# Performance work log

Hardware: AMD Instinct MI355X
Metric: run time of the kernel (lower is better)

The kernel has to match this reference:

```python
import math
import jax, jax.numpy as jnp
import numpy as np

B, S, D, H, L, V = 4, 1024, 1024, 16, 12, 32000
DH = D // H
MAX_LEN = 5000


def _layernorm(x, g, b, eps=1e-5):
    mu = jnp.mean(x, axis=-1, keepdims=True)
    var = jnp.mean(jnp.square(x - mu), axis=-1, keepdims=True)
    return (x - mu) * jax.lax.rsqrt(var + eps) * g + b


def _make_pe():
    pos = np.arange(MAX_LEN, dtype=np.float32)[:, None]
    div = np.exp(np.arange(0, D, 2, dtype=np.float32) * (-math.log(10000.0) / D))
    pe = np.zeros((MAX_LEN, D), dtype=np.float32)
    pe[:, 0::2] = np.sin(pos * div)
    pe[:, 1::2] = np.cos(pos * div)
    return jnp.asarray(pe[:, None, :])  # [max_len, 1, D] as in the torch buffer


def setup_inputs() -> dict:
    key = jax.random.key(0)
    ks = jax.random.split(key, 8)
    X = jax.random.randint(ks[0], (B, S), 0, V)
    emb = jax.random.normal(ks[1], (V, D), dtype=jnp.float32) * 0.02
    pe = _make_pe()
    ln1_g = jnp.ones((L, D), jnp.float32)
    ln1_b = jnp.zeros((L, D), jnp.float32)
    wa = jax.random.normal(ks[2], (L, D, 3 * D), dtype=jnp.float32) * 0.02
    ba = jnp.zeros((L, 3 * D), jnp.float32)
    wp = jax.random.normal(ks[3], (L, D, D), dtype=jnp.float32) * 0.02
    bp = jnp.zeros((L, D), jnp.float32)
    ln2_g = jnp.ones((L, D), jnp.float32)
    ln2_b = jnp.zeros((L, D), jnp.float32)
    wf = jax.random.normal(ks[4], (L, D, D), dtype=jnp.float32) * 0.02
    bf = jnp.zeros((L, D), jnp.float32)
    wout = jax.random.normal(ks[5], (V, D), dtype=jnp.float32) * 0.02
    return dict(X=X, emb=emb, pe=pe, ln1_g=ln1_g, ln1_b=ln1_b, wa=wa, ba=ba,
                wp=wp, bp=bp, ln2_g=ln2_g, ln2_b=ln2_b, wf=wf, bf=bf, wout=wout)


def _block(x, ln1g, ln1b, wa_i, ba_i, wp_i, bp_i, ln2g, ln2b, wf_i, bf_i):
    h = _layernorm(x, ln1g, ln1b)               # post-ln1 value is the residual base
    qkv = h @ wa_i + ba_i                        # [B,S,3D]
    q, k, v = jnp.split(qkv, 3, axis=-1)
    def heads(t):
        return t.reshape(B, S, H, DH).transpose(0, 2, 1, 3)  # [B,H,S,DH]
    q, k, v = heads(q), heads(k), heads(v)
    scores = jnp.einsum('bhqd,bhkd->bhqk', q, k)  # NOTE: no 1/sqrt(d) scaling (scale=False)
    probs = jax.nn.softmax(scores, axis=-1)
    o = jnp.einsum('bhqk,bhkd->bhqd', probs, v)
    o = o.transpose(0, 2, 1, 3).reshape(B, S, D)
    attn_out = o @ wp_i + bp_i
    x = h + attn_out
    x = x + _layernorm(x, ln2g, ln2b) @ wf_i + bf_i
    return x


def reference(X, emb, pe, ln1_g, ln1_b, wa, ba, wp, bp, ln2_g, ln2_b, wf, bf, wout):
    x = emb[X] * math.sqrt(D)           # [B,S,D]
    x = x + pe[:B]                       # faithful: pe indexed by batch dim, broadcast over seq
    for i in range(L):
        x = _block(x, ln1_g[i], ln1_b[i], wa[i], ba[i], wp[i], bp[i],
                   ln2_g[i], ln2_b[i], wf[i], bf[i])
    logits = jnp.einsum('bsd,vd->bsv', x, wout)  # Linear(d, vocab, bias=False)
    return logits
```

## Files before the change

### kernel.cpp

```cpp
#include <hip/hip_runtime.h>
#include <hip/hip_bf16.h>

typedef __attribute__((ext_vector_type(4))) float f32x4;
typedef __attribute__((ext_vector_type(8))) short s16x8;
typedef __attribute__((ext_vector_type(4))) short s16x4;

constexpr int Bc = 4, Sc = 1024, Dc = 1024, Hc = 16, DHc = 64, Lc = 12, Vc = 32000;
constexpr int Tc = Bc * Sc;
constexpr int D3c = 3 * Dc;

static __device__ __forceinline__ short f2bf(float f) {
  union { float f; unsigned u; } v; v.f = f;
  unsigned r = (v.u + 0x7FFFu + ((v.u >> 16) & 1u)) >> 16;
  return (short)r;
}

__launch_bounds__(256)
__global__ void k_embed(const int* __restrict__ X, const float* __restrict__ emb,
                        const float* __restrict__ pe, float* __restrict__ x) {
  int row = blockIdx.x;
  int b = row >> 10;
  int tok = X[row];
  int t = threadIdx.x;
  float4 e = ((const float4*)(emb + (size_t)tok * Dc))[t];
  float4 p = ((const float4*)(pe + (size_t)b * Dc))[t];
  float4 r;
  r.x = e.x * 32.0f + p.x;  r.y = e.y * 32.0f + p.y;
  r.z = e.z * 32.0f + p.z;  r.w = e.w * 32.0f + p.w;
  ((float4*)(x + (size_t)row * Dc))[t] = r;
}

template<bool WF32>
__launch_bounds__(256)
__global__ void k_ln(const float* __restrict__ x, const float* __restrict__ g,
                     const float* __restrict__ be, float* __restrict__ hf,
                     short* __restrict__ hb) {
  int row = blockIdx.x, t = threadIdx.x;
  float4 v = ((const float4*)(x + (size_t)row * Dc))[t];
  float s1 = v.x + v.y + v.z + v.w;
  float s2 = v.x * v.x + v.y * v.y + v.z * v.z + v.w * v.w;
#pragma unroll
  for (int off = 1; off < 64; off <<= 1) {
    s1 += __shfl_xor(s1, off);
    s2 += __shfl_xor(s2, off);
  }
  __shared__ float a1[4], a2[4];
  if ((t & 63) == 0) { a1[t >> 6] = s1; a2[t >> 6] = s2; }
  __syncthreads();
  s1 = a1[0] + a1[1] + a1[2] + a1[3];
  s2 = a2[0] + a2[1] + a2[2] + a2[3];
  float mu = s1 * (1.0f / Dc);
  float var = s2 * (1.0f / Dc) - mu * mu;
  float rs = rsqrtf(var + 1e-5f);
  float4 gg = ((const float4*)g)[t];
  float4 bb = ((const float4*)be)[t];
  float4 r;
  r.x = (v.x - mu) * rs * gg.x + bb.x;
  r.y = (v.y - mu) * rs * gg.y + bb.y;
  r.z = (v.z - mu) * rs * gg.z + bb.z;
  r.w = (v.w - mu) * rs * gg.w + bb.w;
  if (WF32) ((float4*)(hf + (size_t)row * Dc))[t] = r;
  s16x4 o; o[0] = f2bf(r.x); o[1] = f2bf(r.y); o[2] = f2bf(r.z); o[3] = f2bf(r.w);
  ((s16x4*)(hb + (size_t)row * Dc))[t] = o;
}

__launch_bounds__(256)
__global__ void k_transpose_bf(const float* __restrict__ in0, short* __restrict__ out0,
                               int R, int C) {
  const float* in = in0 + (size_t)blockIdx.z * R * C;
  short* out = out0 + (size_t)blockIdx.z * R * C;
  __shared__ float tile[64][65];
  int c0 = blockIdx.x * 64, r0 = blockIdx.y * 64;
  int t = threadIdx.x;
#pragma unroll
  for (int e = 0; e < 16; ++e) {
    int idx = e * 256 + t;
    int r = idx >> 6, c = idx & 63;
    tile[r][c] = in[(size_t)(r0 + r) * C + c0 + c];
  }
  __syncthreads();
#pragma unroll
  for (int e = 0; e < 16; ++e) {
    int idx = e * 256 + t;
    int c = idx >> 6, r = idx & 63;
    out[(size_t)(c0 + c) * R + r0 + r] = f2bf(tile[r][c]);
  }
}

__launch_bounds__(256)
__global__ void k_f2bf(const float* __restrict__ in, short* __restrict__ out, size_t n) {
  size_t i = ((size_t)blockIdx.x * 256 + threadIdx.x) * 4;
  size_t stride = (size_t)gridDim.x * 1024;
  for (; i < n; i += stride) {
    float4 v = *(const float4*)(in + i);
    s16x4 r; r[0] = f2bf(v.x); r[1] = f2bf(v.y); r[2] = f2bf(v.z); r[3] = f2bf(v.w);
    *(s16x4*)(out + i) = r;
  }
}

template<int MODE>
__launch_bounds__(256)
__global__ void k_gemm(const short* __restrict__ A, const short* __restrict__ Bt,
                       const float* __restrict__ bias, const float* __restrict__ res,
                       void* __restrict__ Cout, int M, int N, int K) {
  __shared__ __align__(16) short Al[128][40];
  __shared__ __align__(16) short Bl[128][40];
  int m0 = blockIdx.y * 128, n0 = blockIdx.x * 128;
  int t = threadIdx.x;
  int w = t >> 6, lane = t & 63;
  int wr = w >> 1, wc = w & 1;
  int lg = lane >> 4, lr = lane & 15;
  f32x4 acc[4][4];
#pragma unroll
  for (int i = 0; i < 4; ++i)
#pragma unroll
    for (int j = 0; j < 4; ++j) { acc[i][j][0] = 0.f; acc[i][j][1] = 0.f; acc[i][j][2] = 0.f; acc[i][j][3] = 0.f; }
  int srow = t >> 1, skc = (t & 1) * 16;
  const short* ga = A + (size_t)(m0 + srow) * K + skc;
  const short* gb = Bt + (size_t)(n0 + srow) * K + skc;
  for (int k0 = 0; k0 < K; k0 += 32) {
    s16x8 a0 = *(const s16x8*)(ga + k0);
    s16x8 a1 = *(const s16x8*)(ga + k0 + 8);
    s16x8 b0 = *(const s16x8*)(gb + k0);
    s16x8 b1 = *(const s16x8*)(gb + k0 + 8);
    *(s16x8*)&Al[srow][skc] = a0;
    *(s16x8*)&Al[srow][skc + 8] = a1;
    *(s16x8*)&Bl[srow][skc] = b0;
    *(s16x8*)&Bl[srow][skc + 8] = b1;
    __syncthreads();
    s16x8 af[4], bfr[4];
#pragma unroll
    for (int mi = 0; mi < 4; ++mi) af[mi] = *(const s16x8*)&Al[wr * 64 + mi * 16 + lr][lg * 8];
#pragma unroll
    for (int ni = 0; ni < 4; ++ni) bfr[ni] = *(const s16x8*)&Bl[wc * 64 + ni * 16 + lr][lg * 8];
#pragma unroll
    for (int mi = 0; mi < 4; ++mi)
#pragma unroll
      for (int ni = 0; ni < 4; ++ni)
        acc[mi][ni] = __builtin_amdgcn_mfma_f32_16x16x32_bf16(af[mi], bfr[ni], acc[mi][ni], 0, 0, 0);
    __syncthreads();
  }
#pragma unroll
  for (int mi = 0; mi < 4; ++mi) {
#pragma unroll
    for (int ni = 0; ni < 4; ++ni) {
      int ncol = n0 + wc * 64 + ni * 16 + lr;
      float bv = (MODE == 2) ? 0.0f : bias[ncol];
      int mbase = m0 + wr * 64 + mi * 16 + lg * 4;
#pragma unroll
      for (int j = 0; j < 4; ++j) {
        size_t idx = (size_t)(mbase + j) * N + ncol;
        float vv = acc[mi][ni][j] + bv;
        if (MODE == 1) vv += res[idx];
        if (MODE == 0) ((short*)Cout)[idx] = f2bf(vv);
        else           ((float*)Cout)[idx] = vv;
      }
    }
  }
}

__launch_bounds__(256)
__global__ void k_attn(const short* __restrict__ qkv, short* __restrict__ obf) {
  int bh = blockIdx.x;
  int b = bh >> 4, h = bh & 15;
  int q0 = blockIdx.y * 64;
  int t = threadIdx.x, w = t >> 6, lane = t & 63;
  int lg = lane >> 4, lr = lane & 15;
  __shared__ __align__(16) short vls[64][72];
  __shared__ __align__(16) short pls[64][72];
  s16x8 qf0, qf1;
  {
    const short* qp = qkv + (size_t)(b * Sc + q0 + w * 16 + lr) * D3c + h * DHc + lg * 8;
    qf0 = *(const s16x8*)qp;
    qf1 = *(const s16x8*)(qp + 32);
  }
  float mrow[4], lrow[4];
  f32x4 oacc[4];
#pragma unroll
  for (int j = 0; j < 4; ++j) { mrow[j] = -1e30f; lrow[j] = 0.0f; }
#pragma unroll
  for (int f = 0; f < 4; ++f) { oacc[f][0] = 0.f; oacc[f][1] = 0.f; oacc[f][2] = 0.f; oacc[f][3] = 0.f; }

  int vsk = t >> 2, vdh = (t & 3) * 16;
  const short* vbase = qkv + (size_t)(b * Sc) * D3c + 2 * Dc + h * DHc;
  const short* kbase = qkv + (size_t)(b * Sc) * D3c + Dc + h * DHc;

  for (int kt = 0; kt < Sc / 64; ++kt) {
    int k0 = kt * 64;
    __syncthreads();
    {
      const short* vp = vbase + (size_t)(k0 + vsk) * D3c + vdh;
      s16x8 v0 = *(const s16x8*)vp;
      s16x8 v1 = *(const s16x8*)(vp + 8);
#pragma unroll
      for (int e = 0; e < 8; ++e) vls[vdh + e][vsk] = v0[e];
#pragma unroll
      for (int e = 0; e < 8; ++e) vls[vdh + 8 + e][vsk] = v1[e];
    }
    __syncthreads();
    f32x4 sc[4];
#pragma unroll
    for (int f = 0; f < 4; ++f) {
      const short* kp = kbase + (size_t)(k0 + f * 16 + lr) * D3c + lg * 8;
      s16x8 kf0 = *(const s16x8*)kp;
      s16x8 kf1 = *(const s16x8*)(kp + 32);
      f32x4 c; c[0] = 0.f; c[1] = 0.f; c[2] = 0.f; c[3] = 0.f;
      c = __builtin_amdgcn_mfma_f32_16x16x32_bf16(qf0, kf0, c, 0, 0, 0);
      c = __builtin_amdgcn_mfma_f32_16x16x32_bf16(qf1, kf1, c, 0, 0, 0);
      sc[f] = c;
    }
#pragma unroll
    for (int j = 0; j < 4; ++j) {
      float mx = fmaxf(fmaxf(sc[0][j], sc[1][j]), fmaxf(sc[2][j], sc[3][j]));
#pragma unroll
      for (int off = 1; off < 16; off <<= 1) mx = fmaxf(mx, __shfl_xor(mx, off));
      float mn = fmaxf(mrow[j], mx);
      float scale = __expf(mrow[j] - mn);
      mrow[j] = mn;
      float s = 0.0f;
#pragma unroll
      for (int f = 0; f < 4; ++f) {
        float pv = __expf(sc[f][j] - mn);
        sc[f][j] = pv;
        s += pv;
      }
#pragma unroll
      for (int off = 1; off < 16; off <<= 1) s += __shfl_xor(s, off);
      lrow[j] = lrow[j] * scale + s;
#pragma unroll
      for (int f = 0; f < 4; ++f) oacc[f][j] *= scale;
    }
#pragma unroll
    for (int f = 0; f < 4; ++f)
#pragma unroll
      for (int j = 0; j < 4; ++j)
        pls[w * 16 + lg * 4 + j][f * 16 + lr] = f2bf(sc[f][j]);
    __syncthreads();
    s16x8 pa0 = *(const s16x8*)&pls[w * 16 + lr][lg * 8];
    s16x8 pa1 = *(const s16x8*)&pls[w * 16 + lr][32 + lg * 8];
#pragma unroll
    for (int f = 0; f < 4; ++f) {
      s16x8 vb0 = *(const s16x8*)&vls[f * 16 + lr][lg * 8];
      s16x8 vb1 = *(const s16x8*)&vls[f * 16 + lr][32 + lg * 8];
      oacc[f] = __builtin_amdgcn_mfma_f32_16x16x32_bf16(pa0, vb0, oacc[f], 0, 0, 0);
      oacc[f] = __builtin_amdgcn_mfma_f32_16x16x32_bf16(pa1, vb1, oacc[f], 0, 0, 0);
    }
  }
#pragma unroll
  for (int j = 0; j < 4; ++j) {
    float inv = 1.0f / lrow[j];
    int srow = q0 + w * 16 + lg * 4 + j;
#pragma unroll
    for (int f = 0; f < 4; ++f)
      obf[(size_t)(b * Sc + srow) * Dc + h * DHc + f * 16 + lr] = f2bf(oacc[f][j] * inv);
  }
}

extern "C" void kernel_launch(void* const* d_in, const int* in_sizes, int n_in,
                              void* d_out, int out_size, void* d_ws, size_t ws_size,
                              hipStream_t stream) {
  const int*   X    = (const int*)d_in[0];
  const float* emb  = (const float*)d_in[1];
  const float* pe   = (const float*)d_in[2];
  const float* ln1g = (const float*)d_in[3];
  const float* ln1b = (const float*)d_in[4];
  const float* wa   = (const float*)d_in[5];
  const float* ba   = (const float*)d_in[6];
  const float* wp   = (const float*)d_in[7];
  const float* bp   = (const float*)d_in[8];
  const float* ln2g = (const float*)d_in[9];
  const float* ln2b = (const float*)d_in[10];
  const float* wf   = (const float*)d_in[11];
  const float* bfv  = (const float*)d_in[12];
  const float* wout = (const float*)d_in[13];
  float* out = (float*)d_out;

  char* p = (char*)d_ws;
  float* x    = (float*)p; p += (size_t)Tc * Dc * 4;
  float* hx   = (float*)p; p += (size_t)Tc * Dc * 4;
  short* hbf  = (short*)p; p += (size_t)Tc * Dc * 2;
  short* l2bf = (short*)p; p += (size_t)Tc * Dc * 2;
  short* qkvb = (short*)p; p += (size_t)Tc * D3c * 2;
  short* obf  = (short*)p; p += (size_t)Tc * Dc * 2;
  short* xbf  = (short*)p; p += (size_t)Tc * Dc * 2;
  short* wat  = (short*)p; p += (size_t)Lc * D3c * Dc * 2;
  short* wpt  = (short*)p; p += (size_t)Lc * Dc * Dc * 2;
  short* wft  = (short*)p; p += (size_t)Lc * Dc * Dc * 2;
  short* woutb = (short*)p; p += (size_t)Vc * Dc * 2;

  k_transpose_bf<<<dim3(D3c / 64, Dc / 64, Lc), 256, 0, stream>>>(wa, wat, Dc, D3c);
  k_transpose_bf<<<dim3(Dc / 64, Dc / 64, Lc), 256, 0, stream>>>(wp, wpt, Dc, Dc);
  k_transpose_bf<<<dim3(Dc / 64, Dc / 64, Lc), 256, 0, stream>>>(wf, wft, Dc, Dc);
  k_f2bf<<<4096, 256, 0, stream>>>(wout, woutb, (size_t)Vc * Dc);

  k_embed<<<Tc, 256, 0, stream>>>(X, emb, pe, x);

  for (int l = 0; l < Lc; ++l) {
    k_ln<true><<<Tc, 256, 0, stream>>>(x, ln1g + l * Dc, ln1b + l * Dc, hx, hbf);
    k_gemm<0><<<dim3(D3c / 128, Tc / 128), 256, 0, stream>>>(
        hbf, wat + (size_t)l * D3c * Dc, ba + l * D3c, nullptr, qkvb, Tc, D3c, Dc);
    k_attn<<<dim3(Bc * Hc, Sc / 64), 256, 0, stream>>>(qkvb, obf);
    k_gemm<1><<<dim3(Dc / 128, Tc / 128), 256, 0, stream>>>(
        obf, wpt + (size_t)l * Dc * Dc, bp + l * Dc, hx, x, Tc, Dc, Dc);
    k_ln<false><<<Tc, 256, 0, stream>>>(x, ln2g + l * Dc, ln2b + l * Dc, nullptr, l2bf);
    k_gemm<1><<<dim3(Dc / 128, Tc / 128), 256, 0, stream>>>(
        l2bf, wft + (size_t)l * Dc * Dc, bfv + l * Dc, x, x, Tc, Dc, Dc);
  }

  k_f2bf<<<2048, 256, 0, stream>>>(x, xbf, (size_t)Tc * Dc);
  k_gemm<2><<<dim3(Vc / 128, Tc / 128), 256, 0, stream>>>(
      xbf, woutb, nullptr, nullptr, out, Tc, Vc, Dc);
}
```

Baseline: 3.672 ms.

## Use direct global-to-LDS loads, XOR-swizzled LDS, BK=64 and XCD block remap in GEMM

```diff
diff --git a/kernel.cpp b/kernel.cpp
--- a/kernel.cpp
+++ b/kernel.cpp
@@ -98,46 +98,71 @@
   }
 }
 
-template<int MODE>
+template<int MODE, bool SWZ>
 __launch_bounds__(256)
 __global__ void k_gemm(const short* __restrict__ A, const short* __restrict__ Bt,
                        const float* __restrict__ bias, const float* __restrict__ res,
-                       void* __restrict__ Cout, int M, int N, int K) {
-  __shared__ __align__(16) short Al[128][40];
-  __shared__ __align__(16) short Bl[128][40];
-  int m0 = blockIdx.y * 128, n0 = blockIdx.x * 128;
+                       void* __restrict__ Cout, int M, int N, int K, int nby) {
+  __shared__ __align__(16) short Al[128][64];
+  __shared__ __align__(16) short Bl[128][64];
+  int bid = blockIdx.x;
+  if (SWZ) {
+    int nwg = gridDim.x;
+    int q = nwg >> 3, r = nwg & 7;
+    int xcd = bid & 7, off = bid >> 3;
+    bid = (xcd < r ? xcd * (q + 1) : r * (q + 1) + (xcd - r) * q) + off;
+  }
+  int by = bid % nby;
+  int bx = bid / nby;
+  int m0 = by * 128, n0 = bx * 128;
   int t = threadIdx.x;
   int w = t >> 6, lane = t & 63;
   int wr = w >> 1, wc = w & 1;
   int lg = lane >> 4, lr = lane & 15;
+
+  int srow = t >> 3, sg = t & 7;
+  int scol = ((sg ^ (srow & 7)) * 8);
+  const short* ga = A + (size_t)(m0 + srow) * K + scol;
+  const short* gb = Bt + (size_t)(n0 + srow) * K + scol;
+  short* la = &Al[srow][sg * 8];
+  short* lb = &Bl[srow][sg * 8];
+
   f32x4 acc[4][4];
 #pragma unroll
   for (int i = 0; i < 4; ++i)
 #pragma unroll
     for (int j = 0; j < 4; ++j) { acc[i][j][0] = 0.f; acc[i][j][1] = 0.f; acc[i][j][2] = 0.f; acc[i][j][3] = 0.f; }
-  int srow = t >> 1, skc = (t & 1) * 16;
-  const short* ga = A + (size_t)(m0 + srow) * K + skc;
-  const short* gb = Bt + (size_t)(n0 + srow) * K + skc;
-  for (int k0 = 0; k0 < K; k0 += 32) {
-    s16x8 a0 = *(const s16x8*)(ga + k0);
-    s16x8 a1 = *(const s16x8*)(ga + k0 + 8);
-    s16x8 b0 = *(const s16x8*)(gb + k0);
-    s16x8 b1 = *(const s16x8*)(gb + k0 + 8);
-    *(s16x8*)&Al[srow][skc] = a0;
-    *(s16x8*)&Al[srow][skc + 8] = a1;
-    *(s16x8*)&Bl[srow][skc] = b0;
-    *(s16x8*)&Bl[srow][skc + 8] = b1;
-    __syncthreads();
-    s16x8 af[4], bfr[4];
-#pragma unroll
-    for (int mi = 0; mi < 4; ++mi) af[mi] = *(const s16x8*)&Al[wr * 64 + mi * 16 + lr][lg * 8];
-#pragma unroll
-    for (int ni = 0; ni < 4; ++ni) bfr[ni] = *(const s16x8*)&Bl[wc * 64 + ni * 16 + lr][lg * 8];
-#pragma unroll
-    for (int mi = 0; mi < 4; ++mi)
-#pragma unroll
-      for (int ni = 0; ni < 4; ++ni)
-        acc[mi][ni] = __builtin_amdgcn_mfma_f32_16x16x32_bf16(af[mi], bfr[ni], acc[mi][ni], 0, 0, 0);
+
+  for (int k0 = 0; k0 < K; k0 += 64) {
+#pragma unroll
+    for (int i = 0; i < 4; ++i) {
+      __builtin_amdgcn_global_load_lds(
+          (const __attribute__((address_space(1))) void*)(ga + (size_t)(i * 32) * K + k0),
+          (__attribute__((address_space(3))) void*)(la + i * 32 * 64), 16, 0, 0);
+      __builtin_amdgcn_global_load_lds(
+          (const __attribute__((address_space(1))) void*)(gb + (size_t)(i * 32) * K + k0),
+          (__attribute__((address_space(3))) void*)(lb + i * 32 * 64), 16, 0, 0);
+    }
+    __syncthreads();
+#pragma unroll
+    for (int kk = 0; kk < 2; ++kk) {
+      s16x8 af[4], bfr[4];
+#pragma unroll
+      for (int mi = 0; mi < 4; ++mi) {
+        int row = wr * 64 + mi * 16 + lr;
+        af[mi] = *(const s16x8*)&Al[row][((kk * 4 + lg) ^ (lr & 7)) * 8];
+      }
+#pragma unroll
+      for (int ni = 0; ni < 4; ++ni) {
+        int row = wc * 64 + ni * 16 + lr;
+        bfr[ni] = *(const s16x8*)&Bl[row][((kk * 4 + lg) ^ (lr & 7)) * 8];
+      }
+#pragma unroll
+      for (int mi = 0; mi < 4; ++mi)
+#pragma unroll
+        for (int ni = 0; ni < 4; ++ni)
+          acc[mi][ni] = __builtin_amdgcn_mfma_f32_16x16x32_bf16(af[mi], bfr[ni], acc[mi][ni], 0, 0, 0);
+    }
     __syncthreads();
   }
 #pragma unroll
@@ -295,19 +320,20 @@
 
   k_embed<<<Tc, 256, 0, stream>>>(X, emb, pe, x);
 
+  const int nby = Tc / 128;
   for (int l = 0; l < Lc; ++l) {
     k_ln<true><<<Tc, 256, 0, stream>>>(x, ln1g + l * Dc, ln1b + l * Dc, hx, hbf);
-    k_gemm<0><<<dim3(D3c / 128, Tc / 128), 256, 0, stream>>>(
-        hbf, wat + (size_t)l * D3c * Dc, ba + l * D3c, nullptr, qkvb, Tc, D3c, Dc);
+    k_gemm<0, false><<<(D3c / 128) * nby, 256, 0, stream>>>(
+        hbf, wat + (size_t)l * D3c * Dc, ba + l * D3c, nullptr, qkvb, Tc, D3c, Dc, nby);
     k_attn<<<dim3(Bc * Hc, Sc / 64), 256, 0, stream>>>(qkvb, obf);
-    k_gemm<1><<<dim3(Dc / 128, Tc / 128), 256, 0, stream>>>(
-        obf, wpt + (size_t)l * Dc * Dc, bp + l * Dc, hx, x, Tc, Dc, Dc);
+    k_gemm<1, false><<<(Dc / 128) * nby, 256, 0, stream>>>(
+        obf, wpt + (size_t)l * Dc * Dc, bp + l * Dc, hx, x, Tc, Dc, Dc, nby);
     k_ln<false><<<Tc, 256, 0, stream>>>(x, ln2g + l * Dc, ln2b + l * Dc, nullptr, l2bf);
-    k_gemm<1><<<dim3(Dc / 128, Tc / 128), 256, 0, stream>>>(
-        l2bf, wft + (size_t)l * Dc * Dc, bfv + l * Dc, x, x, Tc, Dc, Dc);
+    k_gemm<1, false><<<(Dc / 128) * nby, 256, 0, stream>>>(
+        l2bf, wft + (size_t)l * Dc * Dc, bfv + l * Dc, x, x, Tc, Dc, Dc, nby);
   }
 
   k_f2bf<<<2048, 256, 0, stream>>>(x, xbf, (size_t)Tc * Dc);
-  k_gemm<2><<<dim3(Vc / 128, Tc / 128), 256, 0, stream>>>(
-      xbf, woutb, nullptr, nullptr, out, Tc, Vc, Dc);
-}
+  k_gemm<2, true><<<(Vc / 128) * nby, 256, 0, stream>>>(
+      xbf, woutb, nullptr, nullptr, out, Tc, Vc, Dc, nby);
+}
```

Result: no change. 3.633 ms (-1.1%).
